# Optimization experiments

Measured on AMD Instinct MI355X. Metric: run time of the kernel, lower is better.

Reference implementation:

```python
import jax, jax.numpy as jnp
import numpy as np

STRIDE = 8.0

def setup_inputs() -> dict:
    key = jax.random.key(0)
    x = jax.random.normal(key, (16, 340, 76, 76), dtype=jnp.float32)
    # all_mask_anchors: anchor (w,h) in pixels divided by stride (grid units)
    masked_anchors = jnp.array([[10., 13.], [16., 30.], [33., 23.], [30., 61.]], dtype=jnp.float32) / STRIDE
    return {"x": x, "masked_anchors": masked_anchors}

def reference(x, masked_anchors):
    # Eval-mode YOLO anchor decode: returns pred_box of shape (bs, n_anchors*fy*fx, 5+n_classes)
    bs, C, fy, fx = x.shape
    na = masked_anchors.shape[0]
    nc = C // na  # 5 + n_classes
    out = x.reshape(bs, na, nc, fy, fx).transpose(0, 1, 3, 4, 2)  # (bs, na, fy, fx, nc)
    xy = jax.nn.sigmoid(out[..., :2])
    wh = out[..., 2:4]
    rest = jax.nn.sigmoid(out[..., 4:])  # obj + class logits -> probs
    fx_f = jnp.asarray(fx, x.dtype)
    fy_f = jnp.asarray(fy, x.dtype)
    x_shift = jnp.arange(fx, dtype=x.dtype)[None, None, None, :]
    y_shift = jnp.arange(fy, dtype=x.dtype)[None, None, :, None]
    # normalized coords then rescaled by stride*fs (as in pred_box)
    px = (xy[..., 0] + x_shift) / fx_f * (STRIDE * fx_f)
    py = (xy[..., 1] + y_shift) / fy_f * (STRIDE * fy_f)
    pw = jnp.exp(wh[..., 0]) * masked_anchors[None, :, None, None, 0] / fx_f * (STRIDE * fx_f)
    ph = jnp.exp(wh[..., 1]) * masked_anchors[None, :, None, None, 1] / fy_f * (STRIDE * fy_f)
    pred_box = jnp.concatenate(
        [px[..., None], py[..., None], pw[..., None], ph[..., None], rest], axis=-1)
    return pred_box.reshape(bs, -1, nc)
```

## Files before the change

### kernel.cpp

```cpp
#include <hip/hip_runtime.h>
#include <hip/hip_bf16.h>


constexpr int BS = 16;
constexpr int NA = 4;
constexpr int NC = 85;
constexpr int FY = 76;
constexpr int FX = 76;
constexpr int PLANE = FY * FX;
constexpr int TILE  = NC * FX;
constexpr int RV    = FX / 4;
constexpr int NV    = NC * RV;
constexpr int NTHR  = 512;
constexpr int FULL  = 3 * NTHR;
constexpr int TAIL  = NV - FULL;
constexpr float STRIDE_F = 8.0f;
constexpr float LOG2E = 1.4426950408889634f;

__device__ __forceinline__ float fast_sigmoid(float v) {
    return __builtin_amdgcn_rcpf(1.0f + __builtin_amdgcn_exp2f(v * -LOG2E));
}
__device__ __forceinline__ float fast_exp(float v) {
    return __builtin_amdgcn_exp2f(v * LOG2E);
}

__global__ __launch_bounds__(NTHR)
void yolo_decode_kernel(const float* __restrict__ x,
                        const float* __restrict__ anchors,
                        float* __restrict__ out) {
    __shared__ float lds[TILE];

    const int blk = blockIdx.x;
    const int y   = blk % FY;
    const int ba  = blk / FY;
    const int a   = ba % NA;

    const float ax = anchors[a * 2 + 0] * STRIDE_F;
    const float ay = anchors[a * 2 + 1] * STRIDE_F;
    const float yf = (float)y;

    const float* __restrict__ inbase = x + (size_t)ba * NC * PLANE + (size_t)y * FX;
    const int t = threadIdx.x;

    float4 v[4];
    #pragma unroll
    for (int k = 0; k < 3; ++k) {
        const int i = t + NTHR * k;
        const int c = i / RV;
        const int j = i - c * RV;
        v[k] = *(const float4*)(inbase + (size_t)c * PLANE + j * 4);
    }
    if (t < TAIL) {
        const int i = FULL + t;
        const int c = i / RV;
        const int j = i - c * RV;
        v[3] = *(const float4*)(inbase + (size_t)c * PLANE + j * 4);
    }

    #pragma unroll
    for (int k = 0; k < 4; ++k) {
        if (k < 3 || t < TAIL) {
            const int i = (k < 3) ? (t + NTHR * k) : (FULL + t);
            const int c = i / RV;
            const int j = i - c * RV;
            const float vv[4] = {v[k].x, v[k].y, v[k].z, v[k].w};
            float* __restrict__ dst = &lds[(4 * j) * NC + c];
            if (c >= 4) {
                #pragma unroll
                for (int kk = 0; kk < 4; ++kk)
                    dst[kk * NC] = fast_sigmoid(vv[kk]);
            } else if (c == 0) {
                #pragma unroll
                for (int kk = 0; kk < 4; ++kk)
                    dst[kk * NC] = fast_sigmoid(vv[kk]) * STRIDE_F
                                 + (float)(4 * j + kk) * STRIDE_F;
            } else if (c == 1) {
                #pragma unroll
                for (int kk = 0; kk < 4; ++kk)
                    dst[kk * NC] = fast_sigmoid(vv[kk]) * STRIDE_F + yf * STRIDE_F;
            } else if (c == 2) {
                #pragma unroll
                for (int kk = 0; kk < 4; ++kk)
                    dst[kk * NC] = fast_exp(vv[kk]) * ax;
            } else {
                #pragma unroll
                for (int kk = 0; kk < 4; ++kk)
                    dst[kk * NC] = fast_exp(vv[kk]) * ay;
            }
        }
    }

    __syncthreads();

    const float4* __restrict__ ldsv = (const float4*)lds;
    float4* __restrict__ ov = (float4*)(out + (size_t)blk * TILE);
    #pragma unroll
    for (int k = 0; k < 3; ++k)
        ov[t + NTHR * k] = ldsv[t + NTHR * k];
    if (t < TAIL)
        ov[FULL + t] = ldsv[FULL + t];
}

extern "C" void kernel_launch(void* const* d_in, const int* in_sizes, int n_in,
                              void* d_out, int out_size, void* d_ws, size_t ws_size,
                              hipStream_t stream) {
    const float* x       = (const float*)d_in[0];
    const float* anchors = (const float*)d_in[1];
    float* out           = (float*)d_out;

    const int nblocks = BS * NA * FY;
    yolo_decode_kernel<<<nblocks, NTHR, 0, stream>>>(x, anchors, out);
}
```

Baseline: 49.78 us.

## Process two rows per block and remap block IDs across XCDs

Each block now handles two consecutive y rows, so every channel contributes a contiguous 152-float chunk and the block count is halved. Block indices are remapped so that consecutive logical tiles are spread across the eight XCDs, aiming at better L2 locality and load balance. LDS per block doubles to about 51 KB, which limits occupancy to fewer resident blocks per CU, and each thread now holds about seven float4 values in registers.

```diff
diff --git a/kernel.cpp b/kernel.cpp
--- a/kernel.cpp
+++ b/kernel.cpp
@@ -9,11 +9,15 @@
 constexpr int FX = 76;
 constexpr int PLANE = FY * FX;
 constexpr int TILE  = NC * FX;
-constexpr int RV    = FX / 4;
-constexpr int NV    = NC * RV;
+constexpr int YG    = 2;
+constexpr int CHUNK = YG * FX;
+constexpr int RVC   = CHUNK / 4;
+constexpr int NV2   = NC * RVC;
 constexpr int NTHR  = 512;
-constexpr int FULL  = 3 * NTHR;
-constexpr int TAIL  = NV - FULL;
+constexpr int KFULL = NV2 / NTHR;
+constexpr int TAIL2 = NV2 - KFULL * NTHR;
+constexpr int NBLK  = BS * NA * (FY / YG);
+constexpr int PER_XCD = NBLK / 8;
 constexpr float STRIDE_F = 8.0f;
 constexpr float LOG2E = 1.4426950408889634f;
 
@@ -24,81 +28,98 @@
     return __builtin_amdgcn_exp2f(v * LOG2E);
 }
 
+__device__ __forceinline__ void xform_scatter(float* __restrict__ lds,
+                                              int c, int j, float4 v,
+                                              float ax, float ay, float y0f) {
+    const float vv[4] = {v.x, v.y, v.z, v.w};
+    const int pos0 = 4 * j;
+    const int ylocal = (j >= RVC / 2) ? 1 : 0;
+    const int xi0 = pos0 - ylocal * FX;
+    float* __restrict__ dst = &lds[pos0 * NC + c];
+    if (c >= 4) {
+        #pragma unroll
+        for (int kk = 0; kk < 4; ++kk)
+            dst[kk * NC] = fast_sigmoid(vv[kk]);
+    } else if (c == 0) {
+        #pragma unroll
+        for (int kk = 0; kk < 4; ++kk)
+            dst[kk * NC] = fast_sigmoid(vv[kk]) * STRIDE_F
+                         + (float)(xi0 + kk) * STRIDE_F;
+    } else if (c == 1) {
+        const float yf = y0f + (float)ylocal;
+        #pragma unroll
+        for (int kk = 0; kk < 4; ++kk)
+            dst[kk * NC] = fast_sigmoid(vv[kk]) * STRIDE_F + yf * STRIDE_F;
+    } else if (c == 2) {
+        #pragma unroll
+        for (int kk = 0; kk < 4; ++kk)
+            dst[kk * NC] = fast_exp(vv[kk]) * ax;
+    } else {
+        #pragma unroll
+        for (int kk = 0; kk < 4; ++kk)
+            dst[kk * NC] = fast_exp(vv[kk]) * ay;
+    }
+}
+
 __global__ __launch_bounds__(NTHR)
 void yolo_decode_kernel(const float* __restrict__ x,
                         const float* __restrict__ anchors,
                         float* __restrict__ out) {
-    __shared__ float lds[TILE];
+    __shared__ float lds[NC * CHUNK];
 
-    const int blk = blockIdx.x;
-    const int y   = blk % FY;
-    const int ba  = blk / FY;
-    const int a   = ba % NA;
+    const int B    = blockIdx.x;
+    const int orig = (B & 7) * PER_XCD + (B >> 3);
+    const int yp   = orig % (FY / YG);
+    const int ba   = orig / (FY / YG);
+    const int a    = ba % NA;
 
-    const float ax = anchors[a * 2 + 0] * STRIDE_F;
-    const float ay = anchors[a * 2 + 1] * STRIDE_F;
-    const float yf = (float)y;
+    const float ax  = anchors[a * 2 + 0] * STRIDE_F;
+    const float ay  = anchors[a * 2 + 1] * STRIDE_F;
+    const float y0f = (float)(YG * yp);
 
-    const float* __restrict__ inbase = x + (size_t)ba * NC * PLANE + (size_t)y * FX;
+    const float* __restrict__ inbase = x + (size_t)ba * NC * PLANE + (size_t)yp * CHUNK;
     const int t = threadIdx.x;
 
-    float4 v[4];
+    float4 v[KFULL + 1];
     #pragma unroll
-    for (int k = 0; k < 3; ++k) {
+    for (int k = 0; k < KFULL; ++k) {
         const int i = t + NTHR * k;
-        const int c = i / RV;
-        const int j = i - c * RV;
+        const int c = i / RVC;
+        const int j = i - c * RVC;
         v[k] = *(const float4*)(inbase + (size_t)c * PLANE + j * 4);
     }
-    if (t < TAIL) {
-        const int i = FULL + t;
-        const int c = i / RV;
-        const int j = i - c * RV;
-        v[3] = *(const float4*)(inbase + (size_t)c * PLANE + j * 4);
+    if (t < TAIL2) {
+        const int i = KFULL * NTHR + t;
+        const int c = i / RVC;
+        const int j = i - c * RVC;
+        v[KFULL] = *(const float4*)(inbase + (size_t)c * PLANE + j * 4);
     }
 
+    asm volatile("" ::: "memory");
+
     #pragma unroll
-    for (int k = 0; k < 4; ++k) {
-        if (k < 3 || t < TAIL) {
-            const int i = (k < 3) ? (t + NTHR * k) : (FULL + t);
-            const int c = i / RV;
-            const int j = i - c * RV;
-            const float vv[4] = {v[k].x, v[k].y, v[k].z, v[k].w};
-            float* __restrict__ dst = &lds[(4 * j) * NC + c];
-            if (c >= 4) {
-                #pragma unroll
-                for (int kk = 0; kk < 4; ++kk)
-                    dst[kk * NC] = fast_sigmoid(vv[kk]);
-            } else if (c == 0) {
-                #pragma unroll
-                for (int kk = 0; kk < 4; ++kk)
-                    dst[kk * NC] = fast_sigmoid(vv[kk]) * STRIDE_F
-                                 + (float)(4 * j + kk) * STRIDE_F;
-            } else if (c == 1) {
-                #pragma unroll
-                for (int kk = 0; kk < 4; ++kk)
-                    dst[kk * NC] = fast_sigmoid(vv[kk]) * STRIDE_F + yf * STRIDE_F;
-            } else if (c == 2) {
-                #pragma unroll
-                for (int kk = 0; kk < 4; ++kk)
-                    dst[kk * NC] = fast_exp(vv[kk]) * ax;
-            } else {
-                #pragma unroll
-                for (int kk = 0; kk < 4; ++kk)
-                    dst[kk * NC] = fast_exp(vv[kk]) * ay;
-            }
-        }
+    for (int k = 0; k < KFULL; ++k) {
+        const int i = t + NTHR * k;
+        const int c = i / RVC;
+        const int j = i - c * RVC;
+        xform_scatter(lds, c, j, v[k], ax, ay, y0f);
+    }
+    if (t < TAIL2) {
+        const int i = KFULL * NTHR + t;
+        const int c = i / RVC;
+        const int j = i - c * RVC;
+        xform_scatter(lds, c, j, v[KFULL], ax, ay, y0f);
     }
 
     __syncthreads();
 
     const float4* __restrict__ ldsv = (const float4*)lds;
-    float4* __restrict__ ov = (float4*)(out + (size_t)blk * TILE);
+    float4* __restrict__ ov = (float4*)(out + (size_t)(ba * FY + YG * yp) * TILE);
     #pragma unroll
-    for (int k = 0; k < 3; ++k)
+    for (int k = 0; k < KFULL; ++k)
         ov[t + NTHR * k] = ldsv[t + NTHR * k];
-    if (t < TAIL)
-        ov[FULL + t] = ldsv[FULL + t];
+    if (t < TAIL2)
+        ov[KFULL * NTHR + t] = ldsv[KFULL * NTHR + t];
 }
 
 extern "C" void kernel_launch(void* const* d_in, const int* in_sizes, int n_in,
@@ -108,6 +129,5 @@
     const float* anchors = (const float*)d_in[1];
     float* out           = (float*)d_out;
 
-    const int nblocks = BS * NA * FY;
-    yolo_decode_kernel<<<nblocks, NTHR, 0, stream>>>(x, anchors, out);
+    yolo_decode_kernel<<<NBLK, NTHR, 0, stream>>>(x, anchors, out);
 }
```

Result: faster. 41.11 us (-17.4%).
